# Performance work log

Measured on AMD Instinct MI355X. Metric: run time of the kernel, lower is better.

## Reference

```python
import jax, jax.numpy as jnp
import numpy as np

B, T, E, D, N, L, NF = 4, 2048, 512, 512, 16, 4, 2048


def setup_inputs() -> dict:
    key = jax.random.key(0)
    ks = jax.random.split(key, 12)
    r = lambda k, s, sc=1.0: jax.random.normal(k, s, dtype=jnp.float32) * sc
    return {
        "text_emb": r(ks[0], (B, T, E)),
        "W_in": r(ks[1], (E, D), 1.0 / np.sqrt(E).astype(np.float32)),
        "b_in": jnp.zeros((D,), jnp.float32),
        "freq_pe": r(ks[2], (NF, D), 0.02),
        # diagonal-SSM (S4D) params per layer, stacked on leading L axis
        "A_log": r(ks[3], (L, D, N), 0.5),
        "B_ssm": r(ks[4], (L, D, N), 0.5),
        "C_ssm": r(ks[5], (L, D, N), 0.5),
        "log_dt": r(ks[6], (L, D), 0.5) - 4.6,  # dt ~ 0.01
        "D_skip": r(ks[7], (L, D), 0.5),
        "ln_f0_scale": jnp.ones((D,), jnp.float32),
        "ln_f0_bias": jnp.zeros((D,), jnp.float32),
        "W_f0": r(ks[8], (D, 1), 1.0 / np.sqrt(D).astype(np.float32)),
        "b_f0": jnp.zeros((1,), jnp.float32),
        "ln_en_scale": jnp.ones((D,), jnp.float32),
        "ln_en_bias": jnp.zeros((D,), jnp.float32),
        "W_en": r(ks[9], (D, 1), 1.0 / np.sqrt(D).astype(np.float32)),
        "b_en": jnp.zeros((1,), jnp.float32),
    }


def _layernorm(x, scale, bias, eps=1e-5):
    mu = jnp.mean(x, axis=-1, keepdims=True)
    var = jnp.mean(jnp.square(x - mu), axis=-1, keepdims=True)
    return (x - mu) * jax.lax.rsqrt(var + eps) * scale + bias


def _s4_layer(h, A_log, Bm, Cm, log_dt, Dsk):
    # h: [B, T, D]; diagonal SSM with ZOH discretization, scanned over T.
    dt = jnp.exp(log_dt)                 # [D]
    A = -jnp.exp(A_log)                  # [D, N], stable (negative real)
    Abar = jnp.exp(dt[:, None] * A)      # [D, N]
    Bbar = (Abar - 1.0) / A * Bm         # [D, N]
    u_t = jnp.transpose(h, (1, 0, 2))    # [T, B, D]
    x0 = jnp.zeros((h.shape[0], h.shape[2], A.shape[1]), h.dtype)  # [B, D, N]

    def step(x, u):
        x = Abar * x + Bbar * u[..., None]          # [B, D, N]
        y = jnp.einsum('bdn,dn->bd', x, Cm)         # readout
        return x, y

    _, ys = jax.lax.scan(step, x0, u_t)             # ys: [T, B, D]
    y = jnp.transpose(ys, (1, 0, 2)) + Dsk * h      # D skip connection
    return h + jax.nn.gelu(y)                       # residual + activation


def _forward(text_emb, W_in, b_in, freq_pe, A_log, B_ssm, C_ssm, log_dt,
             D_skip, ln_f0_scale, ln_f0_bias, W_f0, b_f0,
             ln_en_scale, ln_en_bias, W_en, b_en):
    x = text_emb @ W_in + b_in                      # [B, T, D]
    Tlen = x.shape[1]
    nf = freq_pe.shape[0]
    if nf >= Tlen:                                  # static-shape crop
        freq = freq_pe[:Tlen]
    else:                                           # static-shape edge pad
        pad = jnp.repeat(freq_pe[-1:], Tlen - nf, axis=0)
        freq = jnp.concatenate([freq_pe, pad], axis=0)
    h = x + freq[None, :, :]
    for l in range(A_log.shape[0]):
        h = _s4_layer(h, A_log[l], B_ssm[l], C_ssm[l], log_dt[l], D_skip[l])
    f0 = (_layernorm(h, ln_f0_scale, ln_f0_bias) @ W_f0 + b_f0)[..., 0]
    en = (_layernorm(h, ln_en_scale, ln_en_bias) @ W_en + b_en)[..., 0]
    return f0, en


def reference(text_emb, W_in, b_in, freq_pe, A_log, B_ssm, C_ssm, log_dt,
              D_skip, ln_f0_scale, ln_f0_bias, W_f0, b_f0,
              ln_en_scale, ln_en_bias, W_en, b_en):
    return _forward(text_emb, W_in, b_in, freq_pe, A_log, B_ssm, C_ssm,
                    log_dt, D_skip, ln_f0_scale, ln_f0_bias, W_f0, b_f0,
                    ln_en_scale, ln_en_bias, W_en, b_en)
```

## Files before the change

kernel.cpp:

```cpp
#include <hip/hip_runtime.h>

#define B_   4
#define T_   2048
#define E_   512
#define D_   512
#define N_   16
#define L_   4
#define TCH  8

typedef __bf16 bf16x8 __attribute__((ext_vector_type(8)));
typedef float  f32x4  __attribute__((ext_vector_type(4)));
typedef float  f32x2  __attribute__((ext_vector_type(2)));
typedef unsigned short us8 __attribute__((ext_vector_type(8)));

__device__ __forceinline__ float us2f(unsigned short u) {
    return __uint_as_float(((unsigned int)u) << 16);
}
__device__ __forceinline__ unsigned short f2us(float f) {
    unsigned int u = __float_as_uint(f);
    unsigned int r = (u + 0x7fffu + ((u >> 16) & 1u)) >> 16;
    return (unsigned short)r;
}
__device__ __forceinline__ float ldin(const void* p, int i, unsigned int f) {
    return f ? ((const float*)p)[i] : us2f(((const unsigned short*)p)[i]);
}
__device__ __forceinline__ unsigned int probe_f32(const void* lnfs) {
    return (((const unsigned int*)lnfs)[0] == 0x3F800000u) ? 1u : 0u;
}
__device__ __forceinline__ f32x2 pk_fma(f32x2 a, f32x2 b, f32x2 c) {
    f32x2 d;
    asm("v_pk_fma_f32 %0, %1, %2, %3" : "=v"(d) : "v"(a), "v"(b), "v"(c));
    return d;
}
__device__ __forceinline__ f32x2 pk_mul(f32x2 a, f32x2 b) {
    f32x2 d;
    asm("v_pk_mul_f32 %0, %1, %2" : "=v"(d) : "v"(a), "v"(b));
    return d;
}
template<int CTRL, int RM>
__device__ __forceinline__ f32x2 dpp2(f32x2 v) {
    f32x2 r;
    r[0] = __int_as_float(__builtin_amdgcn_update_dpp(0, __float_as_int(v[0]), CTRL, RM, 0xF, true));
    r[1] = __int_as_float(__builtin_amdgcn_update_dpp(0, __float_as_int(v[1]), CTRL, RM, 0xF, true));
    return r;
}

#define PA    0
#define PB    32768
#define PC    65536
#define PDT   98304
#define PDSK  100352
#define PLFS  102400
#define PLFB  102912
#define PWF   103424
#define PLES  103936
#define PLEB  104448
#define PWEN  104960
#define PSC   105472
#define PRM_N 105474

#define NB_TEXT 2048
#define NB_PRM  413
#define NB_WT   64
#define NB_S4P  128

__global__ __launch_bounds__(256) void prep_kernel(
    const void* X, const void* Win,
    const void* A_log, const void* B_ssm, const void* C_ssm,
    const void* log_dt, const void* D_skip,
    const void* lnfs, const void* lnfb, const void* Wf0,
    const void* lnes, const void* lneb, const void* Wen,
    const void* bf0, const void* ben,
    unsigned short* __restrict__ textc, unsigned short* __restrict__ Wt,
    float* __restrict__ P, float* __restrict__ P2, float* __restrict__ PW) {
    __shared__ float tile[64 * 65];
    unsigned int f = probe_f32(lnfs);
    int bid = blockIdx.x;
    if (bid < NB_TEXT) {
        int i = (bid * 256 + threadIdx.x) * 8;
        if (f) {
            const float* xf = (const float*)X;
            us8 r;
#pragma unroll
            for (int j = 0; j < 8; j++) r[j] = f2us(xf[i + j]);
            *(us8*)(textc + i) = r;
        } else {
            *(us8*)(textc + i) = *(const us8*)((const unsigned short*)X + i);
        }
    } else if (bid < NB_TEXT + NB_PRM) {
        int i = (bid - NB_TEXT) * 256 + threadIdx.x;
        if      (i < PB)     P[i] = ldin(A_log,  i - PA,   f);
        else if (i < PC)     P[i] = ldin(B_ssm,  i - PB,   f);
        else if (i < PDT)    P[i] = ldin(C_ssm,  i - PC,   f);
        else if (i < PDSK)   P[i] = ldin(log_dt, i - PDT,  f);
        else if (i < PLFS)   P[i] = ldin(D_skip, i - PDSK, f);
        else if (i < PLFB)   P[i] = ldin(lnfs,   i - PLFS, f);
        else if (i < PWF)    P[i] = ldin(lnfb,   i - PLFB, f);
        else if (i < PLES)   P[i] = ldin(Wf0,    i - PWF,  f);
        else if (i < PLEB)   P[i] = ldin(lnes,   i - PLES, f);
        else if (i < PWEN)   P[i] = ldin(lneb,   i - PLEB, f);
        else if (i < PSC)    P[i] = ldin(Wen,    i - PWEN, f);
        else if (i == PSC)     P[i] = ldin(bf0, 0, f);
        else if (i == PSC + 1) P[i] = ldin(ben, 0, f);
    } else if (bid < NB_TEXT + NB_PRM + NB_WT) {
        int tb = bid - (NB_TEXT + NB_PRM);
        int d0 = (tb >> 3) * 64, e0 = (tb & 7) * 64;
        int r = threadIdx.x >> 6, i = threadIdx.x & 63;
#pragma unroll
        for (int k = 0; k < 16; k++) {
            int e = k * 4 + r;
            tile[e * 65 + i] = ldin(Win, (e0 + e) * D_ + d0 + i, f);
        }
        __syncthreads();
#pragma unroll
        for (int k = 0; k < 16; k++) {
            int dd = k * 4 + r;
            Wt[(size_t)(d0 + dd) * E_ + e0 + i] = f2us(tile[i * 65 + dd]);
        }
    } else {
        int i = (bid - (NB_TEXT + NB_PRM + NB_WT)) * 256 + threadIdx.x;
        int n = i & 15;
        int ld = i >> 4;
        float dt = __expf(ldin(log_dt, ld, f));
        float A  = -__expf(ldin(A_log, i, f));
        float Ab = __expf(dt * A);
        float Bb = (Ab - 1.f) / A * ldin(B_ssm, i, f);
        float l2M = 11.541560327111707f * dt * A;
        float M   = exp2f(l2M);
        int base = ld * 48 + n;
        P2[base]      = Ab;
        P2[base + 16] = Bb * ldin(C_ssm, i, f);
        P2[base + 32] = exp2f(64.f * l2M);
        float pw = 1.f;
        size_t pb = ((size_t)ld << 10) + n;
#pragma unroll
        for (int k = 0; k < 64; k++) { PW[pb + (k << 4)] = pw; pw *= M; }
    }
}

__global__ __launch_bounds__(256) void gemm_kernel(const unsigned short* __restrict__ X,
                                                   const unsigned short* __restrict__ Wt,
                                                   const void* __restrict__ freq,
                                                   const void* __restrict__ b_in,
                                                   const void* __restrict__ lnfs,
                                                   float* __restrict__ H) {
    __shared__ unsigned short wlds[64 * 264];
    const unsigned int fl = probe_f32(lnfs);
    const int tid = threadIdx.x;
    const int w  = tid >> 6;
    const int ln = tid & 15;
    const int q  = (tid >> 4) & 3;
    const int d0 = blockIdx.x * 64;
    const int t0 = blockIdx.y * 128;
    const int b  = blockIdx.z;

    f32x4 acc[2][4];
#pragma unroll
    for (int i = 0; i < 2; i++)
#pragma unroll
        for (int j = 0; j < 4; j++) { acc[i][j][0]=0.f; acc[i][j][1]=0.f; acc[i][j][2]=0.f; acc[i][j][3]=0.f; }

    const size_t xbase = ((size_t)b * T_ + t0) * E_;

#pragma unroll
    for (int p = 0; p < 2; ++p) {
        if (p) __syncthreads();
#pragma unroll
        for (int it = 0; it < 8; ++it) {
            int flat = it * 256 + tid;
            int d = flat >> 5;
            int e = (flat & 31) << 3;
            bf16x8 v = *(const bf16x8*)(Wt + (size_t)(d0 + d) * E_ + p * 256 + e);
            *(bf16x8*)(wlds + d * 264 + e) = v;
        }
        __syncthreads();
#pragma unroll
        for (int s = 0; s < 8; ++s) {
            const int eo = s * 32 + q * 8;
            bf16x8 bfr[4];
#pragma unroll
            for (int j = 0; j < 4; j++)
                bfr[j] = *(const bf16x8*)(wlds + (j * 16 + ln) * 264 + eo);
#pragma unroll
            for (int sub = 0; sub < 2; ++sub) {
                const int t = w * 32 + sub * 16 + ln;
                bf16x8 afr = *(const bf16x8*)(X + xbase + (size_t)t * E_ + p * 256 + eo);
#pragma unroll
                for (int j = 0; j < 4; j++)
                    acc[sub][j] = __builtin_amdgcn_mfma_f32_16x16x32_bf16(afr, bfr[j], acc[sub][j], 0, 0, 0);
            }
        }
    }
#pragma unroll
    for (int sub = 0; sub < 2; ++sub) {
#pragma unroll
        for (int j = 0; j < 4; j++) {
            int d  = d0 + j * 16 + ln;
            int tb = t0 + w * 32 + sub * 16 + q * 4;
            float bi = ldin(b_in, d, fl);
            f32x4 o;
#pragma unroll
            for (int r4 = 0; r4 < 4; r4++)
                o[r4] = acc[sub][j][r4] + ldin(freq, (tb + r4) * D_ + d, fl) + bi;
            *(f32x4*)(H + ((size_t)b * D_ + d) * T_ + tb) = o;
        }
    }
}

__global__ __launch_bounds__(256) __attribute__((amdgpu_waves_per_eu(4, 4)))
void s4_kernel(float* __restrict__ H, const float* __restrict__ P,
               const float* __restrict__ P2, const float* __restrict__ PW) {
    __shared__ float hstate[2][3][16];
    const int w = threadIdx.x >> 6, lane = threadIdx.x & 63;
    const int row = blockIdx.x;
    const int d = row & (D_ - 1);
    float* gp = H + (size_t)row * T_ + w * 512 + lane * TCH;

    float u[TCH];
#pragma unroll
    for (int k = 0; k < 2; k++) {
        f32x4 v = *(const f32x4*)(gp + k * 4);
        u[k * 4] = v[0]; u[k * 4 + 1] = v[1]; u[k * 4 + 2] = v[2]; u[k * 4 + 3] = v[3];
    }

    for (int l = 0; l < L_; ++l) {
        const float* pp  = P2 + (size_t)((l << 9) + d) * 48;
        const float* pwt = PW + ((size_t)((l << 9) + d) << 10);
        f32x2 b[8];
#pragma unroll
        for (int n = 0; n < 8; n++) { b[n][0] = 0.f; b[n][1] = 0.f; }
        {
            f32x2 Ab[8];
#pragma unroll
            for (int n = 0; n < 8; n++) Ab[n] = *(const f32x2*)(pp + 2 * n);
#pragma unroll
            for (int j = 0; j < TCH; j++) {
                f32x2 u2; u2[0] = u[j]; u2[1] = u[j];
#pragma unroll
                for (int n = 0; n < 8; n++) b[n] = pk_fma(Ab[n], b[n], u2);
            }
        }
        {
            f32x2 M1[8];
#pragma unroll
            for (int n = 0; n < 8; n++) M1[n] = *(const f32x2*)(pwt + 16 + 2 * n);
#pragma unroll
            for (int n = 0; n < 8; n++) b[n] = pk_fma(M1[n], dpp2<0x111, 0xF>(b[n]), b[n]);
#pragma unroll
            for (int n = 0; n < 8; n++) M1[n] = pk_mul(M1[n], M1[n]);
#pragma unroll
            for (int n = 0; n < 8; n++) b[n] = pk_fma(M1[n], dpp2<0x112, 0xF>(b[n]), b[n]);
#pragma unroll
            for (int n = 0; n < 8; n++) M1[n] = pk_mul(M1[n], M1[n]);
#pragma unroll
            for (int n = 0; n < 8; n++) b[n] = pk_fma(M1[n], dpp2<0x114, 0xF>(b[n]), b[n]);
#pragma unroll
            for (int n = 0; n < 8; n++) M1[n] = pk_mul(M1[n], M1[n]);
#pragma unroll
            for (int n = 0; n < 8; n++) b[n] = pk_fma(M1[n], dpp2<0x118, 0xF>(b[n]), b[n]);
        }
        {
            f32x2 w1[8];
            const float* p1 = pwt + (((lane & 15) + 1) << 4);
#pragma unroll
            for (int n = 0; n < 8; n++) w1[n] = *(const f32x2*)(p1 + 2 * n);
#pragma unroll
            for (int n = 0; n < 8; n++) b[n] = pk_fma(w1[n], dpp2<0x142, 0xA>(b[n]), b[n]);
        }
        {
            f32x2 w2[8];
            const float* p2_ = pwt + (((lane & 31) + 1) << 4);
#pragma unroll
            for (int n = 0; n < 8; n++) w2[n] = *(const f32x2*)(p2_ + 2 * n);
#pragma unroll
            for (int n = 0; n < 8; n++) b[n] = pk_fma(w2[n], dpp2<0x143, 0xC>(b[n]), b[n]);
        }
        if (w < 3 && lane == 63) {
#pragma unroll
            for (int n = 0; n < 8; n++)
                *(f32x2*)(&hstate[l & 1][w][2 * n]) = b[n];
        }
        f32x2 z[8];
#pragma unroll
        for (int n = 0; n < 8; n++) z[n] = dpp2<0x138, 0xF>(b[n]);
        __syncthreads();
        if (w) {
            f32x2 E[8];
#pragma unroll
            for (int n = 0; n < 8; n++) E[n] = *(const f32x2*)(&hstate[l & 1][0][2 * n]);
            if (w > 1) {
                f32x2 Msg[8];
#pragma unroll
                for (int n = 0; n < 8; n++) Msg[n] = *(const f32x2*)(pp + 32 + 2 * n);
                for (int k = 1; k < w; ++k) {
#pragma unroll
                    for (int n = 0; n < 8; n++) {
                        f32x2 h0 = *(const f32x2*)(&hstate[l & 1][k][2 * n]);
                        E[n] = pk_fma(Msg[n], E[n], h0);
                    }
                }
            }
            f32x2 wl[8];
            const float* pl = pwt + (lane << 4);
#pragma unroll
            for (int n = 0; n < 8; n++) wl[n] = *(const f32x2*)(pl + 2 * n);
#pragma unroll
            for (int n = 0; n < 8; n++) z[n] = pk_fma(wl[n], E[n], z[n]);
        }
        float Dsk = P[PDSK + l * D_ + d];
        f32x2 Ab[8], CB[8];
#pragma unroll
        for (int n = 0; n < 8; n++) Ab[n] = *(const f32x2*)(pp + 2 * n);
#pragma unroll
        for (int n = 0; n < 8; n++) CB[n] = *(const f32x2*)(pp + 16 + 2 * n);
#pragma unroll
        for (int j = 0; j < TCH; j++) {
            float uu = u[j];
            f32x2 u2; u2[0] = uu; u2[1] = uu;
#pragma unroll
            for (int n = 0; n < 8; n++) z[n] = pk_fma(Ab[n], z[n], u2);
            f32x2 ya; ya[0] = 0.f; ya[1] = 0.f;
            f32x2 yb; yb[0] = 0.f; yb[1] = 0.f;
#pragma unroll
            for (int n = 0; n < 8; n += 2) {
                ya = pk_fma(CB[n], z[n], ya);
                yb = pk_fma(CB[n + 1], z[n + 1], yb);
            }
            f32x2 s = ya + yb;
            float y = fmaf(Dsk, uu, s[0] + s[1]);
            float t  = fmaf(0.044715f, y * y * y, y);
            float em = exp2f(-2.30220818f * t);
            float r  = __builtin_amdgcn_rcpf(1.f + em);
            u[j] = fmaf(y, r, uu);
        }
    }
#pragma unroll
    for (int k = 0; k < 2; k++) {
        f32x4 v;
        v[0] = u[k * 4]; v[1] = u[k * 4 + 1]; v[2] = u[k * 4 + 2]; v[3] = u[k * 4 + 3];
        *(f32x4*)(gp + k * 4) = v;
    }
}

__global__ __launch_bounds__(256) void final_kernel(const float* __restrict__ H,
                                                    const float* __restrict__ P,
                                                    void* __restrict__ out,
                                                    const void* __restrict__ lnfs_raw) {
    __shared__ float red[4][8][64];
    unsigned int f = probe_f32(lnfs_raw);
    int tid = threadIdx.x;
    int w = tid >> 6, tl = tid & 63;
    int tg = blockIdx.x * 64 + tl;
    int b = tg >> 11, t = tg & (T_ - 1);
    float S1=0.f,S2=0.f,Pf=0.f,Pe=0.f,Cf=0.f,Ce=0.f,Df=0.f,De=0.f;
    const float* hp = H + ((size_t)b * D_) * T_ + t;
#pragma unroll 4
    for (int i = 0; i < 128; i++) {
        int d = w * 128 + i;
        float hv = hp[(size_t)d * T_];
        float sf = P[PLFS + d], bfv = P[PLFB + d], wf = P[PWF + d];
        float se = P[PLES + d], bev = P[PLEB + d], we = P[PWEN + d];
        S1 += hv; S2 = fmaf(hv, hv, S2);
        float tf = sf * wf, te = se * we;
        Pf = fmaf(hv, tf, Pf); Pe = fmaf(hv, te, Pe);
        Cf += tf; Ce += te;
        Df = fmaf(bfv, wf, Df); De = fmaf(bev, we, De);
    }
    red[w][0][tl]=S1; red[w][1][tl]=S2; red[w][2][tl]=Pf; red[w][3][tl]=Pe;
    red[w][4][tl]=Cf; red[w][5][tl]=Ce; red[w][6][tl]=Df; red[w][7][tl]=De;
    __syncthreads();
    if (w == 0) {
        float a[8];
#pragma unroll
        for (int k = 0; k < 8; k++)
            a[k] = red[0][k][tl] + red[1][k][tl] + red[2][k][tl] + red[3][k][tl];
        float mu  = a[0] * (1.f / 512.f);
        float var = a[1] * (1.f / 512.f) - mu * mu;
        float r   = rsqrtf(var + 1e-5f);
        float f0  = r * (a[2] - mu * a[4]) + a[6] + P[PSC + 0];
        float en  = r * (a[3] - mu * a[5]) + a[7] + P[PSC + 1];
        if (f) {
            ((float*)out)[tg]           = f0;
            ((float*)out)[B_ * T_ + tg] = en;
        } else {
            ((unsigned short*)out)[tg]           = f2us(f0);
            ((unsigned short*)out)[B_ * T_ + tg] = f2us(en);
        }
    }
}

extern "C" void kernel_launch(void* const* d_in, const int* in_sizes, int n_in,
                              void* d_out, int out_size, void* d_ws, size_t ws_size,
                              hipStream_t stream) {
    (void)in_sizes; (void)n_in; (void)out_size; (void)ws_size;
    float* ws = (float*)d_ws;
    float* P     = ws;
    float* H     = ws + 105504;
    unsigned short* textc = (unsigned short*)(ws + 4299808);
    unsigned short* Wt    = (unsigned short*)(ws + 6396960);
    float* P2    = ws + 6528032;
    float* PW    = ws + 6626336;

    prep_kernel<<<dim3(NB_TEXT + NB_PRM + NB_WT + NB_S4P), dim3(256), 0, stream>>>(
        d_in[0], d_in[1], d_in[4], d_in[5], d_in[6], d_in[7], d_in[8],
        d_in[9], d_in[10], d_in[11], d_in[13], d_in[14], d_in[15],
        d_in[12], d_in[16], textc, Wt, P, P2, PW);
    gemm_kernel<<<dim3(8, 16, 4), dim3(256), 0, stream>>>(textc, Wt, d_in[3], d_in[2], d_in[9], H);
    s4_kernel<<<dim3(2048), dim3(256), 0, stream>>>(H, P, P2, PW);
    final_kernel<<<dim3(128), dim3(256), 0, stream>>>(H, P, d_out, d_in[9]);
}
```

Before: 175.8 us.

## Map one wavefront per SSM row with 32-step chunks, drop cross-wave LDS combine

The S4 scan kernel now assigns one full (b,d) row to each wavefront, with each lane handling 32 timesteps instead of 8. This removes the shared-memory state exchange, the block barrier and the serial cross-wave carry fix-up. The in-row prefix combine now loads precomputed decay powers from the PW table instead of squaring them on the fly. In exchange, each lane runs a longer sequential chunk and needs more registers, and the grid shrinks to 512 blocks, which cuts the number of waves available to hide latency.

```diff
diff --git a/kernel.cpp b/kernel.cpp
--- a/kernel.cpp
+++ b/kernel.cpp
@@ -6,7 +6,7 @@
 #define D_   512
 #define N_   16
 #define L_   4
-#define TCH  8
+#define TCH  32
 
 typedef __bf16 bf16x8 __attribute__((ext_vector_type(8)));
 typedef float  f32x4  __attribute__((ext_vector_type(4)));
@@ -30,11 +30,6 @@
 __device__ __forceinline__ f32x2 pk_fma(f32x2 a, f32x2 b, f32x2 c) {
     f32x2 d;
     asm("v_pk_fma_f32 %0, %1, %2, %3" : "=v"(d) : "v"(a), "v"(b), "v"(c));
-    return d;
-}
-__device__ __forceinline__ f32x2 pk_mul(f32x2 a, f32x2 b) {
-    f32x2 d;
-    asm("v_pk_mul_f32 %0, %1, %2" : "=v"(d) : "v"(a), "v"(b));
     return d;
 }
 template<int CTRL, int RM>
@@ -42,6 +37,13 @@
     f32x2 r;
     r[0] = __int_as_float(__builtin_amdgcn_update_dpp(0, __float_as_int(v[0]), CTRL, RM, 0xF, true));
     r[1] = __int_as_float(__builtin_amdgcn_update_dpp(0, __float_as_int(v[1]), CTRL, RM, 0xF, true));
+    return r;
+}
+template<int CTRL>
+__device__ __forceinline__ f32x2 mdpp2(f32x2 v) {
+    f32x2 r;
+    r[0] = __int_as_float(__builtin_amdgcn_mov_dpp(__float_as_int(v[0]), CTRL, 0xF, 0xF, true));
+    r[1] = __int_as_float(__builtin_amdgcn_mov_dpp(__float_as_int(v[1]), CTRL, 0xF, 0xF, true));
     return r;
 }
 
@@ -125,12 +127,11 @@
         float A  = -__expf(ldin(A_log, i, f));
         float Ab = __expf(dt * A);
         float Bb = (Ab - 1.f) / A * ldin(B_ssm, i, f);
-        float l2M = 11.541560327111707f * dt * A;
+        float l2M = 46.166241308446827f * dt * A;
         float M   = exp2f(l2M);
-        int base = ld * 48 + n;
+        int base = ld * 32 + n;
         P2[base]      = Ab;
         P2[base + 16] = Bb * ldin(C_ssm, i, f);
-        P2[base + 32] = exp2f(64.f * l2M);
         float pw = 1.f;
         size_t pb = ((size_t)ld << 10) + n;
 #pragma unroll
@@ -207,24 +208,23 @@
     }
 }
 
-__global__ __launch_bounds__(256) __attribute__((amdgpu_waves_per_eu(4, 4)))
+__global__ __launch_bounds__(256, 2)
 void s4_kernel(float* __restrict__ H, const float* __restrict__ P,
                const float* __restrict__ P2, const float* __restrict__ PW) {
-    __shared__ float hstate[2][3][16];
     const int w = threadIdx.x >> 6, lane = threadIdx.x & 63;
-    const int row = blockIdx.x;
+    const int row = blockIdx.x * 4 + w;
     const int d = row & (D_ - 1);
-    float* gp = H + (size_t)row * T_ + w * 512 + lane * TCH;
+    float* gp = H + (size_t)row * T_ + lane * TCH;
 
     float u[TCH];
 #pragma unroll
-    for (int k = 0; k < 2; k++) {
+    for (int k = 0; k < TCH / 4; k++) {
         f32x4 v = *(const f32x4*)(gp + k * 4);
         u[k * 4] = v[0]; u[k * 4 + 1] = v[1]; u[k * 4 + 2] = v[2]; u[k * 4 + 3] = v[3];
     }
 
     for (int l = 0; l < L_; ++l) {
-        const float* pp  = P2 + (size_t)((l << 9) + d) * 48;
+        const float* pp  = P2 + (size_t)((l << 9) + d) * 32;
         const float* pwt = PW + ((size_t)((l << 9) + d) << 10);
         f32x2 b[8];
 #pragma unroll
@@ -241,23 +241,23 @@
             }
         }
         {
-            f32x2 M1[8];
-#pragma unroll
-            for (int n = 0; n < 8; n++) M1[n] = *(const f32x2*)(pwt + 16 + 2 * n);
-#pragma unroll
-            for (int n = 0; n < 8; n++) b[n] = pk_fma(M1[n], dpp2<0x111, 0xF>(b[n]), b[n]);
-#pragma unroll
-            for (int n = 0; n < 8; n++) M1[n] = pk_mul(M1[n], M1[n]);
-#pragma unroll
-            for (int n = 0; n < 8; n++) b[n] = pk_fma(M1[n], dpp2<0x112, 0xF>(b[n]), b[n]);
-#pragma unroll
-            for (int n = 0; n < 8; n++) M1[n] = pk_mul(M1[n], M1[n]);
-#pragma unroll
-            for (int n = 0; n < 8; n++) b[n] = pk_fma(M1[n], dpp2<0x114, 0xF>(b[n]), b[n]);
-#pragma unroll
-            for (int n = 0; n < 8; n++) M1[n] = pk_mul(M1[n], M1[n]);
-#pragma unroll
-            for (int n = 0; n < 8; n++) b[n] = pk_fma(M1[n], dpp2<0x118, 0xF>(b[n]), b[n]);
+            f32x2 W[8];
+#pragma unroll
+            for (int n = 0; n < 8; n++) W[n] = *(const f32x2*)(pwt + 16 + 2 * n);
+#pragma unroll
+            for (int n = 0; n < 8; n++) b[n] = pk_fma(W[n], mdpp2<0x111>(b[n]), b[n]);
+#pragma unroll
+            for (int n = 0; n < 8; n++) W[n] = *(const f32x2*)(pwt + 32 + 2 * n);
+#pragma unroll
+            for (int n = 0; n < 8; n++) b[n] = pk_fma(W[n], mdpp2<0x112>(b[n]), b[n]);
+#pragma unroll
+            for (int n = 0; n < 8; n++) W[n] = *(const f32x2*)(pwt + 64 + 2 * n);
+#pragma unroll
+            for (int n = 0; n < 8; n++) b[n] = pk_fma(W[n], mdpp2<0x114>(b[n]), b[n]);
+#pragma unroll
+            for (int n = 0; n < 8; n++) W[n] = *(const f32x2*)(pwt + 128 + 2 * n);
+#pragma unroll
+            for (int n = 0; n < 8; n++) b[n] = pk_fma(W[n], mdpp2<0x118>(b[n]), b[n]);
         }
         {
             f32x2 w1[8];
@@ -275,38 +275,9 @@
 #pragma unroll
             for (int n = 0; n < 8; n++) b[n] = pk_fma(w2[n], dpp2<0x143, 0xC>(b[n]), b[n]);
         }
-        if (w < 3 && lane == 63) {
-#pragma unroll
-            for (int n = 0; n < 8; n++)
-                *(f32x2*)(&hstate[l & 1][w][2 * n]) = b[n];
-        }
         f32x2 z[8];
 #pragma unroll
-        for (int n = 0; n < 8; n++) z[n] = dpp2<0x138, 0xF>(b[n]);
-        __syncthreads();
-        if (w) {
-            f32x2 E[8];
-#pragma unroll
-            for (int n = 0; n < 8; n++) E[n] = *(const f32x2*)(&hstate[l & 1][0][2 * n]);
-            if (w > 1) {
-                f32x2 Msg[8];
-#pragma unroll
-                for (int n = 0; n < 8; n++) Msg[n] = *(const f32x2*)(pp + 32 + 2 * n);
-                for (int k = 1; k < w; ++k) {
-#pragma unroll
-                    for (int n = 0; n < 8; n++) {
-                        f32x2 h0 = *(const f32x2*)(&hstate[l & 1][k][2 * n]);
-                        E[n] = pk_fma(Msg[n], E[n], h0);
-                    }
-                }
-            }
-            f32x2 wl[8];
-            const float* pl = pwt + (lane << 4);
-#pragma unroll
-            for (int n = 0; n < 8; n++) wl[n] = *(const f32x2*)(pl + 2 * n);
-#pragma unroll
-            for (int n = 0; n < 8; n++) z[n] = pk_fma(wl[n], E[n], z[n]);
-        }
+        for (int n = 0; n < 8; n++) z[n] = mdpp2<0x138>(b[n]);
         float Dsk = P[PDSK + l * D_ + d];
         f32x2 Ab[8], CB[8];
 #pragma unroll
@@ -335,7 +306,7 @@
         }
     }
 #pragma unroll
-    for (int k = 0; k < 2; k++) {
+    for (int k = 0; k < TCH / 4; k++) {
         f32x4 v;
         v[0] = u[k * 4]; v[1] = u[k * 4 + 1]; v[2] = u[k * 4 + 2]; v[3] = u[k * 4 + 3];
         *(f32x4*)(gp + k * 4) = v;
@@ -399,13 +370,13 @@
     unsigned short* textc = (unsigned short*)(ws + 4299808);
     unsigned short* Wt    = (unsigned short*)(ws + 6396960);
     float* P2    = ws + 6528032;
-    float* PW    = ws + 6626336;
+    float* PW    = ws + 6593568;
 
     prep_kernel<<<dim3(NB_TEXT + NB_PRM + NB_WT + NB_S4P), dim3(256), 0, stream>>>(
         d_in[0], d_in[1], d_in[4], d_in[5], d_in[6], d_in[7], d_in[8],
         d_in[9], d_in[10], d_in[11], d_in[13], d_in[14], d_in[15],
         d_in[12], d_in[16], textc, Wt, P, P2, PW);
     gemm_kernel<<<dim3(8, 16, 4), dim3(256), 0, stream>>>(textc, Wt, d_in[3], d_in[2], d_in[9], H);
-    s4_kernel<<<dim3(2048), dim3(256), 0, stream>>>(H, P, P2, PW);
+    s4_kernel<<<dim3(512), dim3(256), 0, stream>>>(H, P, P2, PW);
     final_kernel<<<dim3(128), dim3(256), 0, stream>>>(H, P, d_out, d_in[9]);
 }
```

Measured after the change: 173.9 us. Within noise of the previous version (-1.1%).
